# Kernel tuning notes

Measured on AMD Instinct MI355X. Metric: run time of the kernel, lower is better.

Reference implementation:

```python
import jax, jax.numpy as jnp
import numpy as np

B, N, F_IN, F_HID, F_OUT = 16, 1024, 512, 512, 512


def setup_inputs() -> dict:
    key = jax.random.key(0)
    ks = jax.random.split(key, 8)
    return {
        "batch_graph": jax.random.normal(ks[0], (B, N, F_IN), dtype=jnp.float32),
        "adj": jax.random.uniform(ks[1], (B, N, N), dtype=jnp.float32),
        "W1": jax.random.normal(ks[2], (F_IN, F_HID), dtype=jnp.float32) * (1.0 / np.sqrt(F_IN)),
        "b1": jax.random.normal(ks[3], (F_HID,), dtype=jnp.float32) * 0.02,
        "W2": jax.random.normal(ks[4], (F_HID, F_HID), dtype=jnp.float32) * (1.0 / np.sqrt(F_HID)),
        "b2": jax.random.normal(ks[5], (F_HID,), dtype=jnp.float32) * 0.02,
        "W3": jax.random.normal(ks[6], (F_HID, F_OUT), dtype=jnp.float32) * (1.0 / np.sqrt(F_HID)),
        "b3": jax.random.normal(ks[7], (F_OUT,), dtype=jnp.float32) * 0.02,
    }


def _normalize_adj(adj):
    # torch: adj.sum(1) sums over rows -> per-column sums, shape [B, N]
    colsum = jnp.sum(adj, axis=1)
    r = jnp.where(colsum > 0, colsum ** -0.5, 0.0)  # inf -> 0 as in original
    # (adj @ diag(r)).T @ diag(r)  ==  r[:,None] * adj^T * r[None,:]  (per batch)
    return r[:, :, None] * jnp.swapaxes(adj, 1, 2) * r[:, None, :]


def reference(batch_graph, adj, W1, b1, W2, b2, W3, b3):
    # The original builds a dense (B*N)x(B*N) block-diagonal adjacency; the
    # block-diagonal matmul is mathematically a per-graph batched matmul.
    # Dropout is identity in eval mode.
    a = _normalize_adj(adj)  # [B, N, N]

    def layer(x, W, b):
        return jnp.einsum('bij,bjf->bif', a, x @ W) + b

    x = jax.nn.relu(layer(batch_graph, W1, b1))
    x = jax.nn.relu(layer(x, W2, b2))
    return layer(x, W3, b3)  # [B, N, F_OUT]
```

## Files before the change

kernel.cpp:

```cpp
#include <hip/hip_runtime.h>
#include <hip/hip_bf16.h>

typedef __bf16 bf16;
typedef __bf16 bf16x4 __attribute__((ext_vector_type(4)));
typedef __bf16 bf16x8 __attribute__((ext_vector_type(8)));
typedef float f32x4 __attribute__((ext_vector_type(4)));

#define B_ 16
#define N_ 1024
#define F_ 512

__device__ __forceinline__ float rdv(const void* p, size_t i, int f32) {
  return f32 ? ((const float*)p)[i] : (float)((const bf16*)p)[i];
}

__device__ __forceinline__ void gld16(const bf16* g, bf16* l) {
  __builtin_amdgcn_global_load_lds(
      (const __attribute__((address_space(1))) unsigned int*)g,
      (__attribute__((address_space(3))) unsigned int*)l, 16, 0, 0);
}

__global__ void k_detect(const unsigned* __restrict__ w, int* __restrict__ flag) {
  __shared__ int red[256];
  const int t = threadIdx.x;
  int c = 0;
  for (int i = t; i < 4096; i += 256) c += (((w[i] >> 7) & 0xFFu) >= 130u) ? 1 : 0;
  red[t] = c;
  __syncthreads();
  for (int s = 128; s > 0; s >>= 1) {
    if (t < s) red[t] += red[t + s];
    __syncthreads();
  }
  if (t == 0) flag[0] = (red[0] > 100) ? 1 : 0;
}

__global__ void k_prep(const void* b1, const void* b2, const void* b3,
                       const void* W1, const void* W2, const void* W3,
                       const void* X, const int* __restrict__ flag,
                       float* __restrict__ bc, bf16* __restrict__ Wt,
                       bf16* __restrict__ xc) {
  __shared__ float tile[32][33];
  const int bid = blockIdx.x;
  const int t = threadIdx.x;
  const int f = flag[0];
  if (bid < 6) {
    const int j = bid * 256 + t;
    const void* src = (j < 512) ? b1 : (j < 1024 ? b2 : b3);
    bc[j] = rdv(src, (size_t)(j & 511), f);
  } else if (bid < 774) {
    const int bid2 = bid - 6;
    const int z = bid2 >> 8, ti = bid2 & 255;
    const int f0 = (ti & 15) * 32, k0 = (ti >> 4) * 32;
    const int tx = t & 31, ty = t >> 5;
    const void* W = (z == 0) ? W1 : ((z == 1) ? W2 : W3);
    bf16* dst = Wt + (size_t)z * F_ * F_;
#pragma unroll
    for (int s = 0; s < 4; ++s)
      tile[ty + 8 * s][tx] = rdv(W, (size_t)(k0 + ty + 8 * s) * F_ + f0 + tx, f);
    __syncthreads();
#pragma unroll
    for (int s = 0; s < 4; ++s)
      dst[(size_t)(f0 + ty + 8 * s) * F_ + k0 + tx] = (bf16)tile[tx][ty + 8 * s];
  } else {
    const size_t i4 = ((size_t)(bid - 774) * 256 + t) * 4;
    if (f) {
      f32x4 v = *(const f32x4*)((const float*)X + i4);
      bf16 o[4] = {(bf16)v[0], (bf16)v[1], (bf16)v[2], (bf16)v[3]};
      *(ulong1*)&xc[i4] = *(ulong1*)o;
    } else {
      *(ulong1*)&xc[i4] = *(const ulong1*)((const bf16*)X + i4);
    }
  }
}

__global__ void k_tran(const void* adj, const int* __restrict__ flag,
                       bf16* __restrict__ adjT, float* __restrict__ csp) {
  __shared__ float tile[64][65];
  __shared__ float red[4][64];
  const int tx = threadIdx.x, ty = threadIdx.y;
  const int t = ty * 16 + tx;
  const int b = blockIdx.z, i0 = blockIdx.y * 64, j0 = blockIdx.x * 64;
  const size_t sb = (size_t)b * N_ * N_;
  if (flag[0]) {
    const float* src = (const float*)adj + sb;
#pragma unroll
    for (int s = 0; s < 4; ++s) {
      const int jj = ty + 16 * s;
      f32x4 v = *(const f32x4*)&src[(size_t)(j0 + jj) * N_ + i0 + 4 * tx];
#pragma unroll
      for (int u = 0; u < 4; ++u) tile[jj][4 * tx + u] = v[u];
    }
  } else {
    const bf16* src = (const bf16*)adj + sb;
#pragma unroll
    for (int s = 0; s < 4; ++s) {
      const int jj = ty + 16 * s;
      bf16x4 v = *(const bf16x4*)&src[(size_t)(j0 + jj) * N_ + i0 + 4 * tx];
#pragma unroll
      for (int u = 0; u < 4; ++u) tile[jj][4 * tx + u] = (float)v[u];
    }
  }
  __syncthreads();
  {
    const int cc = t & 63, g = t >> 6;
    float s = 0.f;
#pragma unroll
    for (int r = 0; r < 16; ++r) s += tile[g * 16 + r][cc];
    red[g][cc] = s;
  }
  bf16* dst = adjT + sb;
#pragma unroll
  for (int s = 0; s < 4; ++s) {
    const int ii = ty + 16 * s;
    bf16x4 o;
#pragma unroll
    for (int u = 0; u < 4; ++u) o[u] = (bf16)tile[4 * tx + u][ii];
    *(bf16x4*)&dst[(size_t)(i0 + ii) * N_ + j0 + 4 * tx] = o;
  }
  __syncthreads();
  if (t < 64)
    csp[((size_t)(j0 >> 6) * B_ + b) * N_ + i0 + t] =
        red[0][t] + red[1][t] + red[2][t] + red[3][t];
}

__device__ __forceinline__ float rscale(const float* __restrict__ csp, int b, int node) {
  float c = 0.f;
#pragma unroll
  for (int z = 0; z < 16; ++z) c += csp[((size_t)z * B_ + b) * N_ + node];
  return c > 0.f ? rsqrtf(c) : 0.f;
}

template <int BIAS, int RELU, int OUTDYN, int SCALEN, int SCALEM, int GX>
__global__ __launch_bounds__(256)
void k_gemm_bt(const bf16* __restrict__ A, const bf16* __restrict__ Bt,
               const float* __restrict__ bias, void* __restrict__ C,
               const int* __restrict__ flag, const float* __restrict__ csp,
               int Nc, int K, long sA, long sB, long sC) {
  __shared__ __align__(16) char smem[65536];
  const int id = blockIdx.x;
  const int xcd = id & 7, p = id >> 3;
  const int bz = xcd * 2 + (p >> 5);
  const int tl = p & 31;
  const int bx = tl % GX, by = tl / GX;

  const int tid = threadIdx.x;
  const int wid = tid >> 6, lane = tid & 63;
  const int wm = wid >> 1, wn = wid & 1;
  const int quad = lane >> 4, l16 = lane & 15;
  const int rl = lane >> 3;
  const int cg8 = ((lane & 7) ^ rl) * 8;
  const int h = l16 & 7;

  const bf16* gA = A + (size_t)bz * sA + (size_t)by * 128 * K;
  const bf16* gB = Bt + (size_t)bz * sB + (size_t)bx * 128 * K;

  f32x4 acc[4][4];
#pragma unroll
  for (int i = 0; i < 4; ++i)
#pragma unroll
    for (int j = 0; j < 4; ++j) acc[i][j] = (f32x4){0.f, 0.f, 0.f, 0.f};

  auto stage = [&](int d, int k0) {
    bf16* As = (bf16*)(smem + d * 32768);
    bf16* Bs = (bf16*)(smem + d * 32768 + 16384);
#pragma unroll
    for (int i = 0; i < 4; ++i) {
      const int r0 = wid * 32 + i * 8;
      gld16(gA + (size_t)(r0 + rl) * K + k0 + cg8, &As[r0 * 64]);
      gld16(gB + (size_t)(r0 + rl) * K + k0 + cg8, &Bs[r0 * 64]);
    }
  };

  stage(0, 0);
  for (int k0 = 0; k0 < K; k0 += 64) {
    const int cur = (k0 >> 6) & 1;
    if (k0 + 64 < K) {
      stage(1 - cur, k0 + 64);
      asm volatile("s_waitcnt vmcnt(8)\n\ts_barrier" ::: "memory");
    } else {
      asm volatile("s_waitcnt vmcnt(0)\n\ts_barrier" ::: "memory");
    }
    const bf16* As = (const bf16*)(smem + cur * 32768);
    const bf16* Bs = (const bf16*)(smem + cur * 32768 + 16384);
#pragma unroll
    for (int s = 0; s < 2; ++s) {
      bf16x8 af[4], bfv[4];
#pragma unroll
      for (int tm = 0; tm < 4; ++tm)
        af[tm] = *(const bf16x8*)&As[(wm * 64 + tm * 16 + l16) * 64 +
                                     (((quad + 4 * s) ^ h) * 8)];
#pragma unroll
      for (int tn = 0; tn < 4; ++tn)
        bfv[tn] = *(const bf16x8*)&Bs[(wn * 64 + tn * 16 + l16) * 64 +
                                      (((quad + 4 * s) ^ h) * 8)];
#pragma unroll
      for (int tm = 0; tm < 4; ++tm)
#pragma unroll
        for (int tn = 0; tn < 4; ++tn)
          acc[tm][tn] =
              __builtin_amdgcn_mfma_f32_16x16x32_bf16(af[tm], bfv[tn], acc[tm][tn], 0, 0, 0);
    }
    asm volatile("s_barrier" ::: "memory");
  }

  float* rsh = (float*)(smem + 37376);
  if (SCALEN || SCALEM) {
    if (tid < 128) {
      const int node = (SCALEM ? by * 128 : bx * 128) + tid;
      rsh[tid] = rscale(csp, bz, node);
    }
    __syncthreads();
  }

  const size_t cb = (size_t)bz * sC;
  const int mb_w = by * 128 + wm * 64;
  const int nb_w = bx * 128 + wn * 64;

  if (OUTDYN) {
    const int of32 = flag[0];
#pragma unroll
    for (int tn = 0; tn < 4; ++tn) {
      const int n = nb_w + tn * 16 + l16;
      float bv = BIAS ? bias[n] : 0.f;
      const float cscale = SCALEN ? rsh[wn * 64 + tn * 16 + l16] : 1.f;
#pragma unroll
      for (int tm = 0; tm < 4; ++tm) {
        const int m0 = mb_w + tm * 16 + quad * 4;
#pragma unroll
        for (int r = 0; r < 4; ++r) {
          float v = acc[tm][tn][r];
          if (SCALEM) v *= rsh[wm * 64 + tm * 16 + quad * 4 + r];
          if (SCALEN) v *= cscale;
          v += bv;
          if (RELU) v = v > 0.f ? v : 0.f;
          const size_t idx = cb + (size_t)(m0 + r) * Nc + n;
          if (of32) ((float*)C)[idx] = v;
          else      ((bf16*)C)[idx] = (bf16)v;
        }
      }
    }
  } else {
    bf16* W = (bf16*)smem + wid * (64 * 72);
#pragma unroll
    for (int tn = 0; tn < 4; ++tn) {
      const int n = nb_w + tn * 16 + l16;
      float bv = BIAS ? bias[n] : 0.f;
      const float cscale = SCALEN ? rsh[wn * 64 + tn * 16 + l16] : 1.f;
#pragma unroll
      for (int tm = 0; tm < 4; ++tm) {
#pragma unroll
        for (int r = 0; r < 4; ++r) {
          float v = acc[tm][tn][r];
          if (SCALEM) v *= rsh[wm * 64 + tm * 16 + quad * 4 + r];
          if (SCALEN) v *= cscale;
          v += bv;
          if (RELU) v = v > 0.f ? v : 0.f;
          W[(tm * 16 + quad * 4 + r) * 72 + tn * 16 + l16] = (bf16)v;
        }
      }
    }
    bf16* gC = (bf16*)C + cb;
#pragma unroll
    for (int i = 0; i < 8; ++i) {
      const int row = i * 8 + rl;
      bf16x8 v = *(const bf16x8*)&W[row * 72 + (lane & 7) * 8];
      *(bf16x8*)&gC[(size_t)(mb_w + row) * Nc + nb_w + (lane & 7) * 8] = v;
    }
  }
}

extern "C" void kernel_launch(void* const* d_in, const int* in_sizes, int n_in,
                              void* d_out, int out_size, void* d_ws, size_t ws_size,
                              hipStream_t stream) {
  char* ws = (char*)d_ws;
  float* csp  = (float*)ws;
  int*  flag  = (int*)(ws + 1048576);
  float* bc   = (float*)(ws + 1048832);
  bf16* adjT  = (bf16*)(ws + 1056768);
  bf16* Wt    = (bf16*)(ws + 1056768 + 33554432);
  bf16* Zt    = (bf16*)(ws + 1056768 + 33554432 + 3 * F_ * F_ * 2);
  bf16* Xc = (bf16*)d_out;

  const long sW = 0;
  const long sX = (long)N_ * F_;
  const long sZ = (long)F_ * N_;
  const long sAn = (long)N_ * N_;

  k_detect<<<1, 256, 0, stream>>>((const unsigned*)d_in[2], flag);
  k_prep<<<774 + (B_ * N_ * F_) / 1024, 256, 0, stream>>>(
      d_in[3], d_in[5], d_in[7], d_in[2], d_in[4], d_in[6], d_in[0], flag, bc, Wt, Xc);
  k_tran<<<dim3(N_ / 64, N_ / 64, B_), dim3(16, 16), 0, stream>>>(d_in[1], flag, adjT, csp);

  k_gemm_bt<0, 0, 0, 1, 0, 8><<<512, 256, 0, stream>>>(Wt,               Xc, nullptr,   Zt, flag, csp, N_, F_, sW, sX, sZ);
  k_gemm_bt<1, 1, 0, 0, 1, 4><<<512, 256, 0, stream>>>(adjT,             Zt, bc,        Xc, flag, csp, F_, N_, sAn, sZ, sX);
  k_gemm_bt<0, 0, 0, 1, 0, 8><<<512, 256, 0, stream>>>(Wt + F_ * F_,     Xc, nullptr,   Zt, flag, csp, N_, F_, sW, sX, sZ);
  k_gemm_bt<1, 1, 0, 0, 1, 4><<<512, 256, 0, stream>>>(adjT,             Zt, bc + 512,  Xc, flag, csp, F_, N_, sAn, sZ, sX);
  k_gemm_bt<0, 0, 0, 1, 0, 8><<<512, 256, 0, stream>>>(Wt + 2 * F_ * F_, Xc, nullptr,   Zt, flag, csp, N_, F_, sW, sX, sZ);
  k_gemm_bt<1, 0, 1, 0, 1, 4><<<512, 256, 0, stream>>>(adjT,             Zt, bc + 1024, d_out, flag, csp, F_, N_, sAn, sZ, sX);
}
```

Before: 267.1 us.

## Enlarge GEMM tiles to 256x128 with 8-wave blocks and MFMA priority barriers

```diff
diff --git a/kernel.cpp b/kernel.cpp
--- a/kernel.cpp
+++ b/kernel.cpp
@@ -131,16 +131,16 @@
 }
 
 template <int BIAS, int RELU, int OUTDYN, int SCALEN, int SCALEM, int GX>
-__global__ __launch_bounds__(256)
+__global__ __launch_bounds__(512, 2)
 void k_gemm_bt(const bf16* __restrict__ A, const bf16* __restrict__ Bt,
                const float* __restrict__ bias, void* __restrict__ C,
                const int* __restrict__ flag, const float* __restrict__ csp,
                int Nc, int K, long sA, long sB, long sC) {
-  __shared__ __align__(16) char smem[65536];
+  __shared__ __align__(16) char smem[98304];
   const int id = blockIdx.x;
   const int xcd = id & 7, p = id >> 3;
-  const int bz = xcd * 2 + (p >> 5);
-  const int tl = p & 31;
+  const int bz = xcd * 2 + (p >> 4);
+  const int tl = p & 15;
   const int bx = tl % GX, by = tl / GX;
 
   const int tid = threadIdx.x;
@@ -151,7 +151,7 @@
   const int cg8 = ((lane & 7) ^ rl) * 8;
   const int h = l16 & 7;
 
-  const bf16* gA = A + (size_t)bz * sA + (size_t)by * 128 * K;
+  const bf16* gA = A + (size_t)bz * sA + (size_t)by * 256 * K;
   const bf16* gB = Bt + (size_t)bz * sB + (size_t)bx * 128 * K;
 
   f32x4 acc[4][4];
@@ -161,59 +161,67 @@
     for (int j = 0; j < 4; ++j) acc[i][j] = (f32x4){0.f, 0.f, 0.f, 0.f};
 
   auto stage = [&](int d, int k0) {
-    bf16* As = (bf16*)(smem + d * 32768);
-    bf16* Bs = (bf16*)(smem + d * 32768 + 16384);
+    bf16* As = (bf16*)(smem + d * 49152);
+    bf16* Bs = (bf16*)(smem + d * 49152 + 32768);
 #pragma unroll
     for (int i = 0; i < 4; ++i) {
       const int r0 = wid * 32 + i * 8;
       gld16(gA + (size_t)(r0 + rl) * K + k0 + cg8, &As[r0 * 64]);
+    }
+#pragma unroll
+    for (int i = 0; i < 2; ++i) {
+      const int r0 = wid * 16 + i * 8;
       gld16(gB + (size_t)(r0 + rl) * K + k0 + cg8, &Bs[r0 * 64]);
     }
   };
 
   stage(0, 0);
-  for (int k0 = 0; k0 < K; k0 += 64) {
-    const int cur = (k0 >> 6) & 1;
-    if (k0 + 64 < K) {
-      stage(1 - cur, k0 + 64);
-      asm volatile("s_waitcnt vmcnt(8)\n\ts_barrier" ::: "memory");
+  const int NT = K >> 6;
+  for (int kt = 0; kt < NT; ++kt) {
+    const int cur = kt & 1;
+    if (kt + 1 < NT) {
+      stage(1 - cur, (kt + 1) << 6);
+      asm volatile("s_waitcnt vmcnt(6)\n\ts_barrier" ::: "memory");
     } else {
       asm volatile("s_waitcnt vmcnt(0)\n\ts_barrier" ::: "memory");
     }
-    const bf16* As = (const bf16*)(smem + cur * 32768);
-    const bf16* Bs = (const bf16*)(smem + cur * 32768 + 16384);
-#pragma unroll
-    for (int s = 0; s < 2; ++s) {
+    const bf16* As = (const bf16*)(smem + cur * 49152);
+    const bf16* Bs = (const bf16*)(smem + cur * 49152 + 32768);
+#pragma unroll
+    for (int kh = 0; kh < 2; ++kh) {
       bf16x8 af[4], bfv[4];
+      const int ko = (((quad + 4 * kh) ^ h) * 8);
 #pragma unroll
       for (int tm = 0; tm < 4; ++tm)
-        af[tm] = *(const bf16x8*)&As[(wm * 64 + tm * 16 + l16) * 64 +
-                                     (((quad + 4 * s) ^ h) * 8)];
+        af[tm] = *(const bf16x8*)&As[(wm * 64 + tm * 16 + l16) * 64 + ko];
 #pragma unroll
       for (int tn = 0; tn < 4; ++tn)
-        bfv[tn] = *(const bf16x8*)&Bs[(wn * 64 + tn * 16 + l16) * 64 +
-                                      (((quad + 4 * s) ^ h) * 8)];
+        bfv[tn] = *(const bf16x8*)&Bs[(wn * 64 + tn * 16 + l16) * 64 + ko];
+      asm volatile("s_barrier\n\ts_waitcnt lgkmcnt(0)" ::: "memory");
+      __builtin_amdgcn_s_setprio(1);
 #pragma unroll
       for (int tm = 0; tm < 4; ++tm)
 #pragma unroll
         for (int tn = 0; tn < 4; ++tn)
           acc[tm][tn] =
               __builtin_amdgcn_mfma_f32_16x16x32_bf16(af[tm], bfv[tn], acc[tm][tn], 0, 0, 0);
-    }
-    asm volatile("s_barrier" ::: "memory");
-  }
-
-  float* rsh = (float*)(smem + 37376);
+      __builtin_amdgcn_s_setprio(0);
+      asm volatile("s_barrier" ::: "memory");
+    }
+  }
+
+  float* rsh = (float*)(smem + 73728);
   if (SCALEN || SCALEM) {
-    if (tid < 128) {
-      const int node = (SCALEM ? by * 128 : bx * 128) + tid;
+    const int nsc = SCALEM ? 256 : 128;
+    if (tid < nsc) {
+      const int node = (SCALEM ? by * 256 : bx * 128) + tid;
       rsh[tid] = rscale(csp, bz, node);
     }
     __syncthreads();
   }
 
   const size_t cb = (size_t)bz * sC;
-  const int mb_w = by * 128 + wm * 64;
+  const int mb_w = by * 256 + wm * 64;
   const int nb_w = bx * 128 + wn * 64;
 
   if (OUTDYN) {
@@ -291,10 +299,10 @@
       d_in[3], d_in[5], d_in[7], d_in[2], d_in[4], d_in[6], d_in[0], flag, bc, Wt, Xc);
   k_tran<<<dim3(N_ / 64, N_ / 64, B_), dim3(16, 16), 0, stream>>>(d_in[1], flag, adjT, csp);
 
-  k_gemm_bt<0, 0, 0, 1, 0, 8><<<512, 256, 0, stream>>>(Wt,               Xc, nullptr,   Zt, flag, csp, N_, F_, sW, sX, sZ);
-  k_gemm_bt<1, 1, 0, 0, 1, 4><<<512, 256, 0, stream>>>(adjT,             Zt, bc,        Xc, flag, csp, F_, N_, sAn, sZ, sX);
-  k_gemm_bt<0, 0, 0, 1, 0, 8><<<512, 256, 0, stream>>>(Wt + F_ * F_,     Xc, nullptr,   Zt, flag, csp, N_, F_, sW, sX, sZ);
-  k_gemm_bt<1, 1, 0, 0, 1, 4><<<512, 256, 0, stream>>>(adjT,             Zt, bc + 512,  Xc, flag, csp, F_, N_, sAn, sZ, sX);
-  k_gemm_bt<0, 0, 0, 1, 0, 8><<<512, 256, 0, stream>>>(Wt + 2 * F_ * F_, Xc, nullptr,   Zt, flag, csp, N_, F_, sW, sX, sZ);
-  k_gemm_bt<1, 0, 1, 0, 1, 4><<<512, 256, 0, stream>>>(adjT,             Zt, bc + 1024, d_out, flag, csp, F_, N_, sAn, sZ, sX);
-}
+  k_gemm_bt<0, 0, 0, 1, 0, 8><<<256, 512, 0, stream>>>(Wt,               Xc, nullptr,   Zt, flag, csp, N_, F_, sW, sX, sZ);
+  k_gemm_bt<1, 1, 0, 0, 1, 4><<<256, 512, 0, stream>>>(adjT,             Zt, bc,        Xc, flag, csp, F_, N_, sAn, sZ, sX);
+  k_gemm_bt<0, 0, 0, 1, 0, 8><<<256, 512, 0, stream>>>(Wt + F_ * F_,     Xc, nullptr,   Zt, flag, csp, N_, F_, sW, sX, sZ);
+  k_gemm_bt<1, 1, 0, 0, 1, 4><<<256, 512, 0, stream>>>(adjT,             Zt, bc + 512,  Xc, flag, csp, F_, N_, sAn, sZ, sX);
+  k_gemm_bt<0, 0, 0, 1, 0, 8><<<256, 512, 0, stream>>>(Wt + 2 * F_ * F_, Xc, nullptr,   Zt, flag, csp, N_, F_, sW, sX, sZ);
+  k_gemm_bt<1, 0, 1, 0, 1, 4><<<256, 512, 0, stream>>>(adjT,             Zt, bc + 1024, d_out, flag, csp, F_, N_, sAn, sZ, sX);
+}
```

Measured after the change: 273.6 us. +2.4%, slower.
